# Performance work log

Hardware: AMD Instinct MI355X
Metric: run time of the kernel (lower is better)

Reference implementation:

```python
import jax, jax.numpy as jnp
import numpy as np
from jax import lax

EPS = 1e-5
K = 3            # FreqFilter kernel size
G = 8            # groups = out_ch // channel_per_group = 64 // 8


def conv2d(x, w, pad):
    return lax.conv_general_dilated(
        x, w, window_strides=(1, 1), padding=[(pad, pad), (pad, pad)],
        dimension_numbers=("NCHW", "OIHW", "NCHW"))


def leaky(x):
    return jnp.where(x >= 0, x, 0.01 * x)


def freq_filter(y, wf, gamma, beta):
    # y: (n, c, h, w) with c = 64
    n, c, h, w = y.shape
    yp = jnp.pad(y, ((0, 0), (0, 0), (1, 1), (1, 1)), mode="reflect")
    sig = conv2d(yp, wf, pad=0)                       # (n, G*K*K, h, w)
    # BatchNorm2d in training mode: batch statistics over (N,H,W)
    mu = sig.mean(axis=(0, 2, 3), keepdims=True)
    var = sig.var(axis=(0, 2, 3), keepdims=True)
    sig = (sig - mu) * lax.rsqrt(var + EPS)
    sig = sig * gamma[None, :, None, None] + beta[None, :, None, None]
    sig = jax.nn.softmax(sig, axis=1)                 # softmax over all G*K*K channels
    sig = sig.reshape(n, G, K * K, h, w)              # channel = g*(K*K) + k
    # kernel = identity (delta at center tap) - sigma
    center = K * K // 2
    delta = jnp.zeros((K * K,), sig.dtype).at[center].set(1.0)
    kernel = delta[None, None, :, None, None] - sig   # (n, G, 9, h, w)
    # im2col patches of the reflect-padded input, unfold ordering (row-major taps)
    patches = jnp.stack(
        [yp[:, :, i:i + h, j:j + w] for i in range(K) for j in range(K)],
        axis=2)                                        # (n, c, 9, h, w)
    patches = patches.reshape(n, G, c // G, K * K, h, w)
    out = jnp.einsum("ngckhw,ngkhw->ngchw", patches, kernel)
    return out.reshape(n, c, h, w)


def hin(x):
    # InstanceNorm2d (affine=False) on first half of channels
    half = x.shape[1] // 2
    a = x[:, :half]
    mu = a.mean(axis=(2, 3), keepdims=True)
    var = a.var(axis=(2, 3), keepdims=True)
    a = (a - mu) * lax.rsqrt(var + EPS)
    return jnp.concatenate([a, x[:, half:]], axis=1)


def setup_inputs() -> dict:
    key = jax.random.key(0)
    ks = jax.random.split(key, 8)
    n, cin, cout, h, w = 4, 64, 64, 256, 256
    return {
        "x": jax.random.normal(ks[0], (n, cin, h, w), jnp.float32),
        "w1": jax.random.normal(ks[1], (cout, cin, 3, 3), jnp.float32) * 0.05,
        "b1": jax.random.normal(ks[2], (cout,), jnp.float32) * 0.01,
        "wf": jax.random.normal(ks[3], (G * K * K, cout, 3, 3), jnp.float32) * 0.06,
        "bn_gamma": jnp.ones((G * K * K,), jnp.float32),
        "bn_beta": jnp.zeros((G * K * K,), jnp.float32),
        "w2": jax.random.normal(ks[4], (cout, cout, 3, 3), jnp.float32) * 0.05,
        "b2": jax.random.normal(ks[5], (cout,), jnp.float32) * 0.01,
        "wr": jax.random.normal(ks[6], (cout, cin, 1, 1), jnp.float32) * 0.1,
        "br": jax.random.normal(ks[7], (cout,), jnp.float32) * 0.01,
    }


def reference(x, w1, b1, wf, bn_gamma, bn_beta, w2, b2, wr, br):
    y = conv2d(x, w1, pad=1) + b1[None, :, None, None]
    y = freq_filter(y, wf, bn_gamma, bn_beta)
    y = leaky(hin(y))
    y = leaky(conv2d(y, w2, pad=1) + b2[None, :, None, None])
    res = conv2d(x, wr, pad=0) + br[None, :, None, None]
    return res + y
```

## Files before the change

### kernel.cpp

```cpp
#include <hip/hip_runtime.h>

typedef unsigned short u16;
typedef __attribute__((ext_vector_type(8))) short bf16x8;
typedef __attribute__((ext_vector_type(16))) float f32x16;
typedef __attribute__((address_space(3))) void lds_void;
typedef __attribute__((address_space(1))) const void gbl_void;

#define NN 4
#define HH 256
#define WW 256
#define PD 258
#define CIN 64
#define EPSV 1e-5f

__device__ __forceinline__ float b2f(u16 x){ union{unsigned u; float f;} q; q.u = ((unsigned)x)<<16; return q.f; }
__device__ __forceinline__ u16 f2b(float f){ union{float f; unsigned u;} q; q.f = f; unsigned r = q.u + 0x7FFF + ((q.u>>16)&1u); return (u16)(r>>16); }
__device__ __forceinline__ float leakyf(float x){ return x >= 0.f ? x : 0.01f*x; }

__global__ void prep_kernel(const float* __restrict__ w1, const float* __restrict__ wf,
                            const float* __restrict__ w2, const float* __restrict__ wr,
                            u16* __restrict__ wB1, u16* __restrict__ wBf,
                            u16* __restrict__ wB2, u16* __restrict__ wBr){
  int idx = blockIdx.x*256 + threadIdx.x;
  if (idx < 36864){
    int e = idx & 7, lane = (idx >> 3) & 63, rest = idx >> 9;
    int tap = rest % 9, rest2 = rest / 9;
    int cg = rest2 & 1, kq = rest2 >> 1;
    int cout = cg*32 + (lane & 31);
    int cin  = kq*16 + (lane >> 5)*8 + e;
    int src = (cout*64 + cin)*9 + tap;
    wB1[idx] = f2b(w1[src]);
    wB2[idx] = f2b(w2[src]);
  }
  if (idx < 55296){
    int e = idx & 7, lane = (idx >> 3) & 63, rest = idx >> 9;
    int tap = rest % 9, rest2 = rest / 9;
    int cg = rest2 % 3, kq = rest2 / 3;
    int cout = cg*32 + (lane & 31);
    int cin  = kq*16 + (lane >> 5)*8 + e;
    float v = (cout < 72) ? wf[(cout*64 + cin)*9 + tap] : 0.f;
    wBf[idx] = f2b(v);
  }
  if (idx < 4096){
    int e = idx & 7, lane = (idx >> 3) & 63, rest = idx >> 9;
    int cg = rest & 1, kq = rest >> 1;
    int cout = cg*32 + (lane & 31);
    int cin  = kq*16 + (lane >> 5)*8 + e;
    wBr[idx] = f2b(wr[cout*64 + cin]);
  }
}

__global__ __launch_bounds__(256) void padx_kernel(const float* __restrict__ x, u16* __restrict__ xpad){
  int n = blockIdx.x >> 8, h = blockIdx.x & 255, t = threadIdx.x;
  u16* dstrow = xpad + ((size_t)(n*PD + h + 1)*PD)*CIN;
  const uint4 z = {0,0,0,0};
  #pragma unroll
  for (int c8 = 0; c8 < 8; ++c8){
    u16 buf[8];
    #pragma unroll
    for (int j = 0; j < 8; ++j)
      buf[j] = f2b(x[((size_t)(n*64 + c8*8 + j))*65536 + h*256 + t]);
    *(uint4*)(dstrow + (size_t)(t+1)*CIN + c8*8) = *(uint4*)buf;
  }
  if (t == 0)   { for (int c8 = 0; c8 < 8; ++c8) *(uint4*)(dstrow + 0*CIN   + c8*8) = z; }
  if (t == 255) { for (int c8 = 0; c8 < 8; ++c8) *(uint4*)(dstrow + 257*CIN + c8*8) = z; }
  if (h == 0 || h == 255){
    u16* brow = xpad + ((size_t)(n*PD + (h == 0 ? 0 : 257))*PD)*CIN;
    for (int p = t; p < PD; p += 256)
      for (int c8 = 0; c8 < 8; ++c8) *(uint4*)(brow + (size_t)p*CIN + c8*8) = z;
  }
}

__global__ void reflect_kernel(u16* __restrict__ y1pad){
  int idx = blockIdx.x*256 + threadIdx.x;
  if (idx >= 4*1028*8) return;
  int n = idx/(1028*8), rem = idx%(1028*8), p = rem >> 3, cc = rem & 7;
  int pr, pc;
  if      (p < 258)  { pr = 0;   pc = p; }
  else if (p < 516)  { pr = 257; pc = p - 258; }
  else if (p < 772)  { pr = 1 + (p - 516); pc = 0; }
  else               { pr = 1 + (p - 772); pc = 257; }
  int sr = (pr == 0) ? 2 : ((pr == 257) ? 255 : pr);
  int sc = (pc == 0) ? 2 : ((pc == 257) ? 255 : pc);
  uint4 v = *(const uint4*)(y1pad + ((size_t)(n*PD + sr)*PD + sc)*CIN + cc*8);
  *(uint4*)(y1pad + ((size_t)(n*PD + pr)*PD + pc)*CIN + cc*8) = v;
}

template<int NCG, int MODE>
__global__ __launch_bounds__(NCG*128, 4) void conv_mfma(
    const u16* __restrict__ Ain, const u16* __restrict__ wB, const float* __restrict__ bias,
    u16* __restrict__ outB, float* __restrict__ outF,
    const u16* __restrict__ xpad, const u16* __restrict__ wBr,
    const float* __restrict__ br,
    float* __restrict__ bnsum, float* __restrict__ bnsumsq){

  constexpr int NC  = (MODE == 1) ? 80 : 64;
  constexpr int NCP = NC + 8;
  constexpr int TPB = NCG*128;
  constexpr int NW  = NCG*2;
  constexpr int RND = (2112 + TPB - 1)/TPB;
  __shared__ __align__(16) char smem[2112*16];

  int t = threadIdx.x, lane = t & 63, wv = t >> 6;
  int l31 = lane & 31, l1 = lane >> 5;
  int cg = wv % NCG, ph = wv / NCG;
  int bid = blockIdx.x;
  int sb = (bid & 7)*256 + (bid >> 3);
  int n = sb >> 9, rem = sb & 511, rowb = rem >> 2, colb = rem & 3;
  int h0 = rowb*2, w0 = colb*64;

  {
    const u16* base = Ain + ((size_t)(n*PD + h0)*PD + w0)*CIN;
    #pragma unroll
    for (int rnd = 0; rnd < RND; ++rnd){
      int c = rnd*TPB + wv*64 + lane;
      if (c < 2112){
        int row = c / 528, rem2 = c - row*528;
        int px = rem2 >> 3, sub = rem2 & 7;
        int subs = sub ^ (px & 7);
        const u16* src = base + (size_t)row*PD*CIN + (size_t)(px*8 + subs)*8;
        __builtin_amdgcn_global_load_lds((gbl_void*)src,
                                         (lds_void*)(smem + (size_t)c*16), 16, 0, 0);
      }
    }
  }
  __syncthreads();

  f32x16 acc[2];
  #pragma unroll
  for (int pg = 0; pg < 2; ++pg)
    #pragma unroll
    for (int i = 0; i < 16; ++i) acc[pg][i] = 0.f;

  #pragma unroll
  for (int kq = 0; kq < 4; ++kq){
    bf16x8 wfr[9];
    #pragma unroll
    for (int tap = 0; tap < 9; ++tap)
      wfr[tap] = *(const bf16x8*)(wB + ((size_t)((kq*NCG + cg)*9 + tap)*64 + lane)*8);
    #pragma unroll
    for (int pg = 0; pg < 2; ++pg){
      #pragma unroll
      for (int tap = 0; tap < 9; ++tap){
        int wrow = ph + tap/3;
        int wcol = pg*32 + l31 + tap%3;
        int chunk = (kq*2 + l1) ^ (wcol & 7);
        bf16x8 afr = *(const bf16x8*)(smem + ((((wrow*66 + wcol) << 3) + chunk) << 4));
        acc[pg] = __builtin_amdgcn_mfma_f32_32x32x16_bf16(afr, wfr[tap], acc[pg], 0, 0, 0);
      }
    }
  }

  int cout = cg*32 + l31;

  if (MODE < 2){
    __syncthreads();
    u16* Bx = (u16*)smem;
    float* bnpart = (float*)(smem + 24576);
    if (MODE == 1){
      float s = 0.f, q = 0.f;
      #pragma unroll
      for (int pg = 0; pg < 2; ++pg)
        #pragma unroll
        for (int reg = 0; reg < 16; ++reg){ float v = acc[pg][reg]; s += v; q += v*v; }
      s += __shfl_xor(s, 32); q += __shfl_xor(q, 32);
      if (l1 == 0){ bnpart[(wv*32 + l31)*2 + 0] = s; bnpart[(wv*32 + l31)*2 + 1] = q; }
    }
    #pragma unroll
    for (int pg = 0; pg < 2; ++pg){
      float bv = (MODE == 0) ? bias[cout] : 0.f;
      #pragma unroll
      for (int reg = 0; reg < 16; ++reg){
        int rowD = (reg & 3) + 8*(reg >> 2) + 4*l1;
        int p = ph*64 + pg*32 + rowD;
        if (MODE == 0 || cout < 80)
          Bx[p*NCP + cout] = f2b(acc[pg][reg] + bv);
      }
    }
    __syncthreads();
    constexpr int nch = NC/8;
    for (int idx = t; idx < 128*nch; idx += TPB){
      int px = idx/nch, c8 = idx - px*nch;
      int rr = px >> 6, cc = px & 63;
      uint4 v = *(const uint4*)(Bx + px*NCP + c8*8);
      if (MODE == 0)
        *(uint4*)(outB + ((size_t)(n*PD + h0 + 1 + rr)*PD + (w0 + 1 + cc))*CIN + c8*8) = v;
      else
        *(uint4*)(outB + ((size_t)(n*65536 + (h0 + rr)*256 + w0 + cc))*80 + c8*8) = v;
    }
    if (MODE == 1 && t < 192){
      int c = t >> 1, which = t & 1;
      if (c < 72){
        int cgf = c >> 5, ci = c & 31;
        float v = bnpart[((cgf*32) + ci)*2 + which] + bnpart[(((NCG + cgf)*32) + ci)*2 + which];
        atomicAdd(which ? &bnsumsq[c] : &bnsum[c], v);
      }
    }
  } else {
    f32x16 racc[2];
    #pragma unroll
    for (int pg = 0; pg < 2; ++pg)
      #pragma unroll
      for (int i = 0; i < 16; ++i) racc[pg][i] = 0.f;
    const u16* Xrow = xpad + ((size_t)(n*PD + h0 + 1 + ph)*PD + (w0 + 1))*CIN;
    #pragma unroll
    for (int kq = 0; kq < 4; ++kq){
      bf16x8 wr8 = *(const bf16x8*)(wBr + ((size_t)((kq*2 + cg)*64 + lane))*8);
      #pragma unroll
      for (int pg = 0; pg < 2; ++pg){
        bf16x8 xfr = *(const bf16x8*)(Xrow + (size_t)(pg*32 + l31)*CIN + kq*16 + l1*8);
        racc[pg] = __builtin_amdgcn_mfma_f32_32x32x16_bf16(xfr, wr8, racc[pg], 0, 0, 0);
      }
    }
    float bv = bias[cout], bb = br[cout];
    float* orow = outF + ((size_t)(n*64 + cout))*65536 + (h0 + ph)*256 + w0;
    #pragma unroll
    for (int pg = 0; pg < 2; ++pg){
      #pragma unroll
      for (int q = 0; q < 4; ++q){
        float4 o;
        o.x = leakyf(acc[pg][q*4+0] + bv) + racc[pg][q*4+0] + bb;
        o.y = leakyf(acc[pg][q*4+1] + bv) + racc[pg][q*4+1] + bb;
        o.z = leakyf(acc[pg][q*4+2] + bv) + racc[pg][q*4+2] + bb;
        o.w = leakyf(acc[pg][q*4+3] + bv) + racc[pg][q*4+3] + bb;
        int px = pg*32 + 8*q + 4*l1;
        *(float4*)(orow + px) = o;
      }
    }
  }
}

__global__ void bnfinal_kernel(const float* __restrict__ bnsum, const float* __restrict__ bnsumsq,
                               const float* __restrict__ gamma, const float* __restrict__ beta,
                               float* __restrict__ bnscale, float* __restrict__ bnshift){
  int c = threadIdx.x;
  if (c < 72){
    const float M = 262144.f;
    float mu  = bnsum[c] / M;
    float var = bnsumsq[c] / M - mu*mu;
    float sc  = gamma[c] * rsqrtf(var + EPSV);
    bnscale[c] = sc;
    bnshift[c] = beta[c] - mu*sc;
  }
}

__global__ __launch_bounds__(256, 4) void filter_kernel(const u16* __restrict__ sig,
                                                        const u16* __restrict__ y1pad,
                                                        const float* __restrict__ bnscale,
                                                        const float* __restrict__ bnshift,
                                                        u16* __restrict__ y2pad,
                                                        float* __restrict__ hinsum,
                                                        float* __restrict__ hinsumsq){
  __shared__ __align__(16) char smem[2112*16];
  __shared__ float sc[72], sh[72];

  int t = threadIdx.x, lane = t & 63, wv = t >> 6;
  if (t < 72){ sc[t] = bnscale[t]; sh[t] = bnshift[t]; }
  int bid = blockIdx.x;
  int sb = (bid & 7)*256 + (bid >> 3);
  int n = sb >> 9, rem = sb & 511, rowb = rem >> 2, colb = rem & 3;
  int h0 = rowb*2, w0 = colb*64;
  int p = t & 127, r = p >> 6, c = p & 63, half = t >> 7;

  {
    const u16* base = y1pad + ((size_t)(n*PD + h0)*PD + w0)*CIN;
    #pragma unroll
    for (int rnd = 0; rnd < 9; ++rnd){
      if (rnd < 8 || wv == 0){
        int cch = rnd*256 + wv*64 + lane;
        int row = cch / 528, rem2 = cch - row*528;
        int px = rem2 >> 3, sub = rem2 & 7;
        int subs = sub ^ (px & 7);
        const u16* src = base + (size_t)row*PD*CIN + (size_t)(px*8 + subs)*8;
        __builtin_amdgcn_global_load_lds((gbl_void*)src,
                                         (lds_void*)(smem + (rnd*256 + wv*64)*16), 16, 0, 0);
      }
    }
  }

  float sv[72];
  const u16* sp = sig + ((size_t)(n*65536 + (h0 + r)*256 + w0 + c))*80;
  #pragma unroll
  for (int i = 0; i < 9; ++i){
    uint4 v = *(const uint4*)(sp + i*8);
    const u16* e = (const u16*)&v;
    #pragma unroll
    for (int j = 0; j < 8; ++j) sv[i*8+j] = b2f(e[j]);
  }
  __syncthreads();
  float mx = -1e30f;
  #pragma unroll
  for (int cc = 0; cc < 72; ++cc){ sv[cc] = sv[cc]*sc[cc] + sh[cc]; mx = fmaxf(mx, sv[cc]); }
  float sum = 0.f;
  #pragma unroll
  for (int cc = 0; cc < 72; ++cc){ sv[cc] = __expf(sv[cc] - mx); sum += sv[cc]; }
  float inv = -1.f/sum;
  float kv[36];
  if (half == 0){
    #pragma unroll
    for (int j = 0; j < 36; ++j) kv[j] = sv[j]*inv;
  } else {
    #pragma unroll
    for (int j = 0; j < 36; ++j) kv[j] = sv[36 + j]*inv;
  }
  #pragma unroll
  for (int c8 = 0; c8 < 4; ++c8) kv[c8*9 + 4] += 1.f;

  float o[32];
  #pragma unroll
  for (int cc = 0; cc < 32; ++cc) o[cc] = 0.f;
  #pragma unroll
  for (int i = 0; i < 3; ++i){
    #pragma unroll
    for (int j = 0; j < 3; ++j){
      int wcol = c + j, wrow = r + i;
      #pragma unroll
      for (int c8 = 0; c8 < 4; ++c8){
        int chunk = half*4 + c8;
        uint4 v = *(const uint4*)(smem + ((((wrow*66 + wcol) << 3) + (chunk ^ (wcol & 7))) << 4));
        const u16* e = (const u16*)&v;
        float k = kv[c8*9 + i*3 + j];
        #pragma unroll
        for (int jj = 0; jj < 8; ++jj) o[c8*8 + jj] = fmaf(k, b2f(e[jj]), o[c8*8 + jj]);
      }
    }
  }
  __syncthreads();

  u16* obuf = (u16*)smem;
  float* ps = (float*)(smem + 20480);
  #pragma unroll
  for (int c8 = 0; c8 < 4; ++c8){
    u16 ob[8];
    #pragma unroll
    for (int jj = 0; jj < 8; ++jj) ob[jj] = f2b(o[c8*8 + jj]);
    *(uint4*)(obuf + p*66 + (half*4 + c8)*8) = *(uint4*)ob;
  }
  __syncthreads();

  {
    int cch = t & 31, seg = t >> 5;
    float s = 0.f, q = 0.f;
    #pragma unroll
    for (int rr = 0; rr < 16; ++rr){
      float v = b2f(obuf[(seg*16 + rr)*66 + cch]);
      s += v; q += v*v;
    }
    ps[(seg*32 + cch)*2 + 0] = s; ps[(seg*32 + cch)*2 + 1] = q;
  }
  for (int idx = t; idx < 1024; idx += 256){
    int pp = idx >> 3, j = idx & 7;
    int rr = pp >> 6, cc = pp & 63;
    uint4 v = *(const uint4*)(obuf + pp*66 + j*8);
    *(uint4*)(y2pad + ((size_t)(n*PD + h0 + 1 + rr)*PD + (w0 + 1 + cc))*CIN + j*8) = v;
  }
  __syncthreads();
  if (t < 64){
    int cc = t >> 1, which = t & 1;
    float v = 0.f;
    #pragma unroll
    for (int seg = 0; seg < 8; ++seg) v += ps[(seg*32 + cc)*2 + which];
    atomicAdd(which ? &hinsumsq[n*32 + cc] : &hinsum[n*32 + cc], v);
  }
}

__global__ void hinfinal_kernel(const float* __restrict__ hinsum, const float* __restrict__ hinsumsq,
                                float* __restrict__ hmu, float* __restrict__ hrs){
  int i = threadIdx.x;
  if (i < 128){
    const float M = 65536.f;
    float mu  = hinsum[i] / M;
    float var = hinsumsq[i] / M - mu*mu;
    hmu[i] = mu;
    hrs[i] = rsqrtf(var + EPSV);
  }
}

__global__ __launch_bounds__(256) void hinapply_kernel(u16* __restrict__ y2pad,
                                                       const float* __restrict__ hmu,
                                                       const float* __restrict__ hrs){
  int n = blockIdx.x / PD, pr = blockIdx.x % PD, t = threadIdx.x;
  u16* row = y2pad + (size_t)(n*PD + pr)*PD*CIN;
  bool ringrow = (pr == 0) || (pr == PD-1);
  for (int idx = t; idx < PD*8; idx += 256){
    int px = idx >> 3, cc = idx & 7;
    uint4* p = (uint4*)(row + (size_t)px*CIN + cc*8);
    if (ringrow || px == 0 || px == PD-1){
      uint4 z = {0,0,0,0}; *p = z; continue;
    }
    uint4 v = *p;
    u16* e = (u16*)&v;
    if (cc < 4){
      int cb = n*32 + cc*8;
      #pragma unroll
      for (int j = 0; j < 8; ++j){
        float f = (b2f(e[j]) - hmu[cb+j]) * hrs[cb+j];
        e[j] = f2b(leakyf(f));
      }
    } else {
      #pragma unroll
      for (int j = 0; j < 8; ++j) e[j] = f2b(leakyf(b2f(e[j])));
    }
    *p = v;
  }
}

extern "C" void kernel_launch(void* const* d_in, const int* in_sizes, int n_in,
                              void* d_out, int out_size, void* d_ws, size_t ws_size,
                              hipStream_t stream){
  const float* x     = (const float*)d_in[0];
  const float* w1    = (const float*)d_in[1];
  const float* b1    = (const float*)d_in[2];
  const float* wf    = (const float*)d_in[3];
  const float* gamma = (const float*)d_in[4];
  const float* beta  = (const float*)d_in[5];
  const float* w2    = (const float*)d_in[6];
  const float* b2    = (const float*)d_in[7];
  const float* wr    = (const float*)d_in[8];
  const float* br    = (const float*)d_in[9];

  char* ws = (char*)d_ws;
  const size_t PADB = (size_t)NN*PD*PD*CIN*2;
  u16* xpad  = (u16*)(ws);
  u16* y1pad = (u16*)(ws + PADB);
  u16* y2pad = (u16*)(ws + 2*PADB);
  float* stats = (float*)(ws + 3*PADB);
  float* bnsum   = stats;        float* bnsumsq = stats + 80;
  float* bnscale = stats + 160;  float* bnshift = stats + 240;
  float* hinsum  = stats + 320;  float* hinsumsq= stats + 448;
  float* hmu     = stats + 576;  float* hrs     = stats + 704;
  u16* wB1 = (u16*)(ws + 3*PADB + 4096);
  u16* wBf = wB1 + 36864;
  u16* wB2 = wBf + 55296;
  u16* wBr = wB2 + 36864;

  u16* sig = (u16*)d_out;
  float* out = (float*)d_out;

  hipMemsetAsync(stats, 0, 4096, stream);
  prep_kernel<<<256, 256, 0, stream>>>(w1, wf, w2, wr, wB1, wBf, wB2, wBr);
  padx_kernel<<<NN*HH, 256, 0, stream>>>(x, xpad);
  conv_mfma<2,0><<<2048, 256, 0, stream>>>(xpad, wB1, b1, y1pad, nullptr, nullptr, nullptr, nullptr, nullptr, nullptr);
  reflect_kernel<<<(4*1028*8 + 255)/256, 256, 0, stream>>>(y1pad);
  conv_mfma<3,1><<<2048, 384, 0, stream>>>(y1pad, wBf, nullptr, sig, nullptr, nullptr, nullptr, nullptr, bnsum, bnsumsq);
  bnfinal_kernel<<<1, 80, 0, stream>>>(bnsum, bnsumsq, gamma, beta, bnscale, bnshift);
  filter_kernel<<<2048, 256, 0, stream>>>(sig, y1pad, bnscale, bnshift, y2pad, hinsum, hinsumsq);
  hinfinal_kernel<<<1, 128, 0, stream>>>(hinsum, hinsumsq, hmu, hrs);
  hinapply_kernel<<<NN*PD, 256, 0, stream>>>(y2pad, hmu, hrs);
  conv_mfma<2,2><<<2048, 256, 0, stream>>>(y2pad, wB2, b2, nullptr, out, xpad, wBr, br, nullptr, nullptr);
}
```

Before: 227.0 us.

## Fuse instance-norm apply and leaky into conv2 LDS tile; shrink sig stride to 72

Removes the separate hinapply pass over y2pad by applying instance-norm normalization, leaky ReLU and zero padding to the conv2 input tile after it is loaded into LDS. The per-image mean/rstd values are staged in shared memory. The sigma intermediate's per-pixel channel stride is also cut from 80 to 72, which reduces write and read traffic between the filter conv and the filter kernel. The cost is redundant elementwise work on halo pixels and an extra LDS pass and barrier inside the conv.

Measured after the change: 218.7 us, median of 2. 3.7% less time.

```diff
diff --git a/kernel.cpp b/kernel.cpp
--- a/kernel.cpp
+++ b/kernel.cpp
@@ -92,14 +92,15 @@
     u16* __restrict__ outB, float* __restrict__ outF,
     const u16* __restrict__ xpad, const u16* __restrict__ wBr,
     const float* __restrict__ br,
-    float* __restrict__ bnsum, float* __restrict__ bnsumsq){
-
-  constexpr int NC  = (MODE == 1) ? 80 : 64;
+    float* __restrict__ bnsum, float* __restrict__ bnsumsq,
+    const float* __restrict__ hmu, const float* __restrict__ hrs){
+
+  constexpr int NC  = (MODE == 1) ? 72 : 64;
   constexpr int NCP = NC + 8;
   constexpr int TPB = NCG*128;
-  constexpr int NW  = NCG*2;
   constexpr int RND = (2112 + TPB - 1)/TPB;
   __shared__ __align__(16) char smem[2112*16];
+  __shared__ float hmr[64];
 
   int t = threadIdx.x, lane = t & 63, wv = t >> 6;
   int l31 = lane & 31, l1 = lane >> 5;
@@ -109,11 +110,13 @@
   int n = sb >> 9, rem = sb & 511, rowb = rem >> 2, colb = rem & 3;
   int h0 = rowb*2, w0 = colb*64;
 
+  if (MODE == 2 && t < 64) hmr[t] = (t < 32) ? hmu[n*32 + t] : hrs[n*32 + (t - 32)];
+
   {
     const u16* base = Ain + ((size_t)(n*PD + h0)*PD + w0)*CIN;
     #pragma unroll
     for (int rnd = 0; rnd < RND; ++rnd){
-      int c = rnd*TPB + wv*64 + lane;
+      int c = rnd*TPB + t;
       if (c < 2112){
         int row = c / 528, rem2 = c - row*528;
         int px = rem2 >> 3, sub = rem2 & 7;
@@ -126,6 +129,38 @@
   }
   __syncthreads();
 
+  if (MODE == 2){
+    #pragma unroll
+    for (int rnd = 0; rnd < RND; ++rnd){
+      int c = rnd*TPB + t;
+      if (c < 2112){
+        int row = c / 528, rem2 = c - row*528;
+        int px = rem2 >> 3, sub = rem2 & 7;
+        int gpr = h0 + row, gpc = w0 + px;
+        uint4* p = (uint4*)(smem + (size_t)c*16);
+        if (gpr == 0 || gpr == 257 || gpc == 0 || gpc == 257){
+          uint4 z = {0,0,0,0}; *p = z;
+        } else {
+          int cg8 = sub ^ (px & 7);
+          uint4 v = *p;
+          u16* e = (u16*)&v;
+          if (cg8 < 4){
+            #pragma unroll
+            for (int j = 0; j < 8; ++j){
+              float f = (b2f(e[j]) - hmr[cg8*8 + j]) * hmr[32 + cg8*8 + j];
+              e[j] = f2b(leakyf(f));
+            }
+          } else {
+            #pragma unroll
+            for (int j = 0; j < 8; ++j) e[j] = f2b(leakyf(b2f(e[j])));
+          }
+          *p = v;
+        }
+      }
+    }
+    __syncthreads();
+  }
+
   f32x16 acc[2];
   #pragma unroll
   for (int pg = 0; pg < 2; ++pg)
@@ -173,7 +208,7 @@
       for (int reg = 0; reg < 16; ++reg){
         int rowD = (reg & 3) + 8*(reg >> 2) + 4*l1;
         int p = ph*64 + pg*32 + rowD;
-        if (MODE == 0 || cout < 80)
+        if (MODE == 0 || cout < 72)
           Bx[p*NCP + cout] = f2b(acc[pg][reg] + bv);
       }
     }
@@ -186,7 +221,7 @@
       if (MODE == 0)
         *(uint4*)(outB + ((size_t)(n*PD + h0 + 1 + rr)*PD + (w0 + 1 + cc))*CIN + c8*8) = v;
       else
-        *(uint4*)(outB + ((size_t)(n*65536 + (h0 + rr)*256 + w0 + cc))*80 + c8*8) = v;
+        *(uint4*)(outB + ((size_t)(n*65536 + (h0 + rr)*256 + w0 + cc))*72 + c8*8) = v;
     }
     if (MODE == 1 && t < 192){
       int c = t >> 1, which = t & 1;
@@ -279,7 +314,7 @@
   }
 
   float sv[72];
-  const u16* sp = sig + ((size_t)(n*65536 + (h0 + r)*256 + w0 + c))*80;
+  const u16* sp = sig + ((size_t)(n*65536 + (h0 + r)*256 + w0 + c))*72;
   #pragma unroll
   for (int i = 0; i < 9; ++i){
     uint4 v = *(const uint4*)(sp + i*8);
@@ -373,35 +408,6 @@
     float var = hinsumsq[i] / M - mu*mu;
     hmu[i] = mu;
     hrs[i] = rsqrtf(var + EPSV);
-  }
-}
-
-__global__ __launch_bounds__(256) void hinapply_kernel(u16* __restrict__ y2pad,
-                                                       const float* __restrict__ hmu,
-                                                       const float* __restrict__ hrs){
-  int n = blockIdx.x / PD, pr = blockIdx.x % PD, t = threadIdx.x;
-  u16* row = y2pad + (size_t)(n*PD + pr)*PD*CIN;
-  bool ringrow = (pr == 0) || (pr == PD-1);
-  for (int idx = t; idx < PD*8; idx += 256){
-    int px = idx >> 3, cc = idx & 7;
-    uint4* p = (uint4*)(row + (size_t)px*CIN + cc*8);
-    if (ringrow || px == 0 || px == PD-1){
-      uint4 z = {0,0,0,0}; *p = z; continue;
-    }
-    uint4 v = *p;
-    u16* e = (u16*)&v;
-    if (cc < 4){
-      int cb = n*32 + cc*8;
-      #pragma unroll
-      for (int j = 0; j < 8; ++j){
-        float f = (b2f(e[j]) - hmu[cb+j]) * hrs[cb+j];
-        e[j] = f2b(leakyf(f));
-      }
-    } else {
-      #pragma unroll
-      for (int j = 0; j < 8; ++j) e[j] = f2b(leakyf(b2f(e[j])));
-    }
-    *p = v;
   }
 }
 
@@ -440,12 +446,11 @@
   hipMemsetAsync(stats, 0, 4096, stream);
   prep_kernel<<<256, 256, 0, stream>>>(w1, wf, w2, wr, wB1, wBf, wB2, wBr);
   padx_kernel<<<NN*HH, 256, 0, stream>>>(x, xpad);
-  conv_mfma<2,0><<<2048, 256, 0, stream>>>(xpad, wB1, b1, y1pad, nullptr, nullptr, nullptr, nullptr, nullptr, nullptr);
+  conv_mfma<2,0><<<2048, 256, 0, stream>>>(xpad, wB1, b1, y1pad, nullptr, nullptr, nullptr, nullptr, nullptr, nullptr, nullptr, nullptr);
   reflect_kernel<<<(4*1028*8 + 255)/256, 256, 0, stream>>>(y1pad);
-  conv_mfma<3,1><<<2048, 384, 0, stream>>>(y1pad, wBf, nullptr, sig, nullptr, nullptr, nullptr, nullptr, bnsum, bnsumsq);
+  conv_mfma<3,1><<<2048, 384, 0, stream>>>(y1pad, wBf, nullptr, sig, nullptr, nullptr, nullptr, nullptr, bnsum, bnsumsq, nullptr, nullptr);
   bnfinal_kernel<<<1, 80, 0, stream>>>(bnsum, bnsumsq, gamma, beta, bnscale, bnshift);
   filter_kernel<<<2048, 256, 0, stream>>>(sig, y1pad, bnscale, bnshift, y2pad, hinsum, hinsumsq);
   hinfinal_kernel<<<1, 128, 0, stream>>>(hinsum, hinsumsq, hmu, hrs);
-  hinapply_kernel<<<NN*PD, 256, 0, stream>>>(y2pad, hmu, hrs);
-  conv_mfma<2,2><<<2048, 256, 0, stream>>>(y2pad, wB2, b2, nullptr, out, xpad, wBr, br, nullptr, nullptr);
-}
+  conv_mfma<2,2><<<2048, 256, 0, stream>>>(y2pad, wB2, b2, nullptr, out, xpad, wBr, br, nullptr, nullptr, hmu, hrs);
+}
```
